# Optimization experiments

Hardware: AMD Instinct MI355X
Metric: run time of the kernel (lower is better)

Reference implementation:

```python
import jax, jax.numpy as jnp
import numpy as np

SEQ, B, IN, H = 1024, 1024, 64, 64

def setup_inputs() -> dict:
    key = jax.random.key(0)
    ks = jax.random.split(key, 6)
    s_in = 1.0 / np.sqrt(IN)
    s_h = 1.0 / np.sqrt(H)
    return {
        "x": jax.random.normal(ks[0], (SEQ, B, IN), dtype=jnp.float32),
        "h": jax.random.normal(ks[1], (1, B, H), dtype=jnp.float32),
        # nn.Linear params: weight (out,in), bias (out,)
        "Wx": jax.random.uniform(ks[2], (H, IN), jnp.float32, -s_in, s_in),
        "bx": jax.random.uniform(ks[3], (H,), jnp.float32, -s_in, s_in),
        "Wh": jax.random.uniform(ks[4], (H, H), jnp.float32, -s_h, s_h),
        "bh": jax.random.uniform(ks[5], (H,), jnp.float32, -s_h, s_h),
    }

def reference(x, h, Wx, bx, Wh, bh):
    act = jnp.tanh  # activation='tanh'
    # Precompute input projection for all timesteps: (S,B,H)
    xp = jnp.einsum('sbi,hi->sbh', x, Wx) + bx
    # lin_h(h).sum(0) with h of shape (1,B,H) == lin_h(h[0])
    h0 = act(jnp.einsum('bj,hj->bh', h[0], Wh) + bh + xp[0])

    def step(h_prev, xt):
        h_new = act(jnp.einsum('bj,hj->bh', h_prev, Wh) + bh + xt)
        return h_new, h_new

    h_last, h_rest = jax.lax.scan(step, h0, xp[1:])
    h_seq = jnp.concatenate([h0[None], h_rest], axis=0)  # (S,B,H)
    return h_seq, h_last
```

## Files before the change

kernel.cpp:

```cpp
#include <hip/hip_runtime.h>
#include <stdint.h>

#define SEQ 1024
#define NB  1024
#define HD  64
#define BH  (NB*HD)
#define RPB 16

typedef _Float16 f16x8 __attribute__((ext_vector_type(8)));
typedef float    f32x4 __attribute__((ext_vector_type(4)));
typedef uint32_t u32x4 __attribute__((ext_vector_type(4)));

#define L2E2 2.8853900817779268f

__device__ __forceinline__ uint32_t pkrtz(float a, float b) {
    auto h = __builtin_amdgcn_cvt_pkrtz(a, b);
    return __builtin_bit_cast(uint32_t, h);
}
__device__ __forceinline__ float tanh_ps(float z) {
    float e = __builtin_amdgcn_exp2f(-__builtin_fabsf(z));
    float a = e + 1.0f;
    float r = __builtin_fmaf(-0.5f, a, 1.45711f);
    r = r * __builtin_fmaf(-a, r, 2.0f);
    r = r * __builtin_fmaf(-a, r, 2.0f);
    float m = __builtin_fmaf(2.0f, r, -1.0f);
    return __builtin_copysignf(m, z);
}
__device__ __forceinline__ void sync_lds() {
    asm volatile("s_waitcnt lgkmcnt(0)" ::: "memory");
    __builtin_amdgcn_s_barrier();
    asm volatile("" ::: "memory");
}

__global__ __launch_bounds__(256, 1) void rnn_kernel(
    const float* __restrict__ x,  const float* __restrict__ h0,
    const float* __restrict__ Wx, const float* __restrict__ bx,
    const float* __restrict__ Wh, const float* __restrict__ bh,
    float* __restrict__ out)
{
    __shared__ uint32_t hw[2][2][4][64];
    __shared__ uint32_t xw[2][2][4][64];

    const int tid  = threadIdx.x;
    const int w    = tid >> 6;
    const int lane = tid & 63;
    const int g    = lane >> 4;
    const int n    = lane & 15;
    const int R0   = blockIdx.x * RPB;
    const size_t row = (size_t)(R0 + n) * HD;
    const size_t xsoff = row + 16 * w + 4 * g;

    f16x8 whA[2], wxA[2];
    #pragma unroll
    for (int T = 0; T < 2; ++T) {
        u32x4 dw, dx;
        #pragma unroll
        for (int q = 0; q < 4; ++q) {
            const int c = 16*q + 4*g + 2*T;
            const float* wp = Wh + (size_t)(16*w + n) * HD + c;
            const float* xr = Wx + (size_t)(16*w + n) * HD + c;
            dw[q] = pkrtz(wp[0]*L2E2, wp[1]*L2E2);
            dx[q] = pkrtz(xr[0]*L2E2, xr[1]*L2E2);
        }
        whA[T] = __builtin_bit_cast(f16x8, dw);
        wxA[T] = __builtin_bit_cast(f16x8, dx);
    }
    f32x4 biasf;
    {
        f32x4 b1 = *(const f32x4*)(bh + 16*w + 4*g);
        f32x4 b2 = *(const f32x4*)(bx + 16*w + 4*g);
        biasf = (b1 + b2) * L2E2;
    }

    {
        f32x4 hv = *(const f32x4*)(h0 + xsoff);
        hw[0][0][w][lane] = pkrtz(hv[0], hv[1]);
        hw[0][1][w][lane] = pkrtz(hv[2], hv[3]);
        f32x4 xv = *(const f32x4*)(x + (size_t)2 * BH + xsoff);
        xw[0][0][w][lane] = pkrtz(xv[0], xv[1]);
        xw[0][1][w][lane] = pkrtz(xv[2], xv[3]);
    }

    f32x4 xp0, xp1;
    #pragma unroll
    for (int s = 0; s < 2; ++s) {
        u32x4 c0, c1;
        #pragma unroll
        for (int q = 0; q < 4; ++q) {
            f32x4 v = *(const f32x4*)(x + (size_t)s * BH + row + 16*q + 4*g);
            c0[q] = pkrtz(v[0], v[1]);
            c1[q] = pkrtz(v[2], v[3]);
        }
        f16x8 f0 = __builtin_bit_cast(f16x8, c0);
        f16x8 f1 = __builtin_bit_cast(f16x8, c1);
        f32x4 tq = __builtin_amdgcn_mfma_f32_16x16x32_f16(wxA[0], f0, biasf, 0, 0, 0);
        f32x4 rv = __builtin_amdgcn_mfma_f32_16x16x32_f16(wxA[1], f1, tq,    0, 0, 0);
        if (s == 0) xp0 = rv; else xp1 = rv;
    }

    f32x4 ring[4];
    ring[3] = *(const f32x4*)(x + (size_t)3 * BH + xsoff);
    ring[0] = *(const f32x4*)(x + (size_t)4 * BH + xsoff);
    ring[1] = *(const f32x4*)(x + (size_t)5 * BH + xsoff);
    ring[2] = *(const f32x4*)(x + (size_t)6 * BH + xsoff);

    const f32x4 zf = {0.f, 0.f, 0.f, 0.f};
    float* optr = out + xsoff;

    sync_lds();

    for (int tb = 0; tb < SEQ; tb += 4) {
        #pragma unroll
        for (int u = 0; u < 4; ++u) {
            const int t = tb + u;
            const int P = u & 1;
            const int Q = (u + 1) & 1;

            u32x4 hc0, hc1, xc0, xc1;
            #pragma unroll
            for (int q = 0; q < 4; ++q) {
                hc0[q] = hw[P][0][q][lane];
                hc1[q] = hw[P][1][q][lane];
                xc0[q] = xw[P][0][q][lane];
                xc1[q] = xw[P][1][q][lane];
            }
            f16x8 fh0 = __builtin_bit_cast(f16x8, hc0);
            f16x8 fh1 = __builtin_bit_cast(f16x8, hc1);
            f16x8 fx0 = __builtin_bit_cast(f16x8, xc0);
            f16x8 fx1 = __builtin_bit_cast(f16x8, xc1);

            f32x4 xpu = (u & 1) ? xp1 : xp0;
            f32x4 pA = __builtin_amdgcn_mfma_f32_16x16x32_f16(whA[0], fh0, xpu, 0, 0, 0);
            f32x4 pB = __builtin_amdgcn_mfma_f32_16x16x32_f16(whA[1], fh1, zf,  0, 0, 0);

            {
                f32x4 tq = __builtin_amdgcn_mfma_f32_16x16x32_f16(wxA[0], fx0, biasf, 0, 0, 0);
                f32x4 rv = __builtin_amdgcn_mfma_f32_16x16x32_f16(wxA[1], fx1, tq,    0, 0, 0);
                if (u & 1) xp1 = rv; else xp0 = rv;
            }

            f32x4 acc = pA + pB;
            f32x4 tv;
            #pragma unroll
            for (int r = 0; r < 4; ++r) tv[r] = tanh_ps(acc[r]);

            hw[Q][0][w][lane] = pkrtz(tv[0], tv[1]);
            hw[Q][1][w][lane] = pkrtz(tv[2], tv[3]);

            {
                f32x4 v = ring[(u + 3) & 3];
                xw[Q][0][w][lane] = pkrtz(v[0], v[1]);
                xw[Q][1][w][lane] = pkrtz(v[2], v[3]);
                int tl = t + 7; tl = tl > SEQ - 1 ? SEQ - 1 : tl;
                ring[(u + 3) & 3] = *(const f32x4*)(x + (size_t)tl * BH + xsoff);
            }

            *(f32x4*)optr = tv;
            if (t == SEQ - 1) *(f32x4*)(optr + BH) = tv;
            optr += BH;

            sync_lds();
        }
    }
}

extern "C" void kernel_launch(void* const* d_in, const int* in_sizes, int n_in,
                              void* d_out, int out_size, void* d_ws, size_t ws_size,
                              hipStream_t stream) {
    const float* x  = (const float*)d_in[0];
    const float* h  = (const float*)d_in[1];
    const float* Wx = (const float*)d_in[2];
    const float* bx = (const float*)d_in[3];
    const float* Wh = (const float*)d_in[4];
    const float* bh = (const float*)d_in[5];
    float* out = (float*)d_out;

    rnn_kernel<<<dim3(NB / RPB), dim3(256), 0, stream>>>(x, h, Wx, bx, Wh, bh, out);
}
```

Baseline: 310.0 us.

## Split recurrence and input-projection into producer/consumer warp groups with LDS handoff

Blocks grow to 512 threads. Four waves run only the recurrent Wh MFMA, tanh and output store. Four producer waves compute the input projection x*Wx+bias ahead of time and pass it through a double-buffered f32 LDS buffer, and the recurrence waves get raised scheduling priority. This removes the Wx MFMAs, x loads and conversions from the critical serial path. The tanh Newton reciprocal is also replaced with a hardware rcp, which costs barrier participation by more waves and an approximate reciprocal.

```diff
diff --git a/kernel.cpp b/kernel.cpp
--- a/kernel.cpp
+++ b/kernel.cpp
@@ -19,10 +19,7 @@
 }
 __device__ __forceinline__ float tanh_ps(float z) {
     float e = __builtin_amdgcn_exp2f(-__builtin_fabsf(z));
-    float a = e + 1.0f;
-    float r = __builtin_fmaf(-0.5f, a, 1.45711f);
-    r = r * __builtin_fmaf(-a, r, 2.0f);
-    r = r * __builtin_fmaf(-a, r, 2.0f);
+    float r = __builtin_amdgcn_rcpf(e + 1.0f);
     float m = __builtin_fmaf(2.0f, r, -1.0f);
     return __builtin_copysignf(m, z);
 }
@@ -32,14 +29,14 @@
     asm volatile("" ::: "memory");
 }
 
-__global__ __launch_bounds__(256, 1) void rnn_kernel(
+__global__ __launch_bounds__(512, 1) void rnn_kernel(
     const float* __restrict__ x,  const float* __restrict__ h0,
     const float* __restrict__ Wx, const float* __restrict__ bx,
     const float* __restrict__ Wh, const float* __restrict__ bh,
     float* __restrict__ out)
 {
     __shared__ uint32_t hw[2][2][4][64];
-    __shared__ uint32_t xw[2][2][4][64];
+    __shared__ __align__(16) f32x4 xpl[2][4][64];
 
     const int tid  = threadIdx.x;
     const int w    = tid >> 6;
@@ -48,118 +45,135 @@
     const int n    = lane & 15;
     const int R0   = blockIdx.x * RPB;
     const size_t row = (size_t)(R0 + n) * HD;
-    const size_t xsoff = row + 16 * w + 4 * g;
 
-    f16x8 whA[2], wxA[2];
-    #pragma unroll
-    for (int T = 0; T < 2; ++T) {
-        u32x4 dw, dx;
+    if (w < 4) {
+        f16x8 whA[2];
         #pragma unroll
-        for (int q = 0; q < 4; ++q) {
-            const int c = 16*q + 4*g + 2*T;
-            const float* wp = Wh + (size_t)(16*w + n) * HD + c;
-            const float* xr = Wx + (size_t)(16*w + n) * HD + c;
-            dw[q] = pkrtz(wp[0]*L2E2, wp[1]*L2E2);
-            dx[q] = pkrtz(xr[0]*L2E2, xr[1]*L2E2);
-        }
-        whA[T] = __builtin_bit_cast(f16x8, dw);
-        wxA[T] = __builtin_bit_cast(f16x8, dx);
-    }
-    f32x4 biasf;
-    {
-        f32x4 b1 = *(const f32x4*)(bh + 16*w + 4*g);
-        f32x4 b2 = *(const f32x4*)(bx + 16*w + 4*g);
-        biasf = (b1 + b2) * L2E2;
-    }
-
-    {
-        f32x4 hv = *(const f32x4*)(h0 + xsoff);
-        hw[0][0][w][lane] = pkrtz(hv[0], hv[1]);
-        hw[0][1][w][lane] = pkrtz(hv[2], hv[3]);
-        f32x4 xv = *(const f32x4*)(x + (size_t)2 * BH + xsoff);
-        xw[0][0][w][lane] = pkrtz(xv[0], xv[1]);
-        xw[0][1][w][lane] = pkrtz(xv[2], xv[3]);
-    }
-
-    f32x4 xp0, xp1;
-    #pragma unroll
-    for (int s = 0; s < 2; ++s) {
-        u32x4 c0, c1;
-        #pragma unroll
-        for (int q = 0; q < 4; ++q) {
-            f32x4 v = *(const f32x4*)(x + (size_t)s * BH + row + 16*q + 4*g);
-            c0[q] = pkrtz(v[0], v[1]);
-            c1[q] = pkrtz(v[2], v[3]);
-        }
-        f16x8 f0 = __builtin_bit_cast(f16x8, c0);
-        f16x8 f1 = __builtin_bit_cast(f16x8, c1);
-        f32x4 tq = __builtin_amdgcn_mfma_f32_16x16x32_f16(wxA[0], f0, biasf, 0, 0, 0);
-        f32x4 rv = __builtin_amdgcn_mfma_f32_16x16x32_f16(wxA[1], f1, tq,    0, 0, 0);
-        if (s == 0) xp0 = rv; else xp1 = rv;
-    }
-
-    f32x4 ring[4];
-    ring[3] = *(const f32x4*)(x + (size_t)3 * BH + xsoff);
-    ring[0] = *(const f32x4*)(x + (size_t)4 * BH + xsoff);
-    ring[1] = *(const f32x4*)(x + (size_t)5 * BH + xsoff);
-    ring[2] = *(const f32x4*)(x + (size_t)6 * BH + xsoff);
-
-    const f32x4 zf = {0.f, 0.f, 0.f, 0.f};
-    float* optr = out + xsoff;
-
-    sync_lds();
-
-    for (int tb = 0; tb < SEQ; tb += 4) {
-        #pragma unroll
-        for (int u = 0; u < 4; ++u) {
-            const int t = tb + u;
-            const int P = u & 1;
-            const int Q = (u + 1) & 1;
-
-            u32x4 hc0, hc1, xc0, xc1;
+        for (int T = 0; T < 2; ++T) {
+            u32x4 dw;
             #pragma unroll
             for (int q = 0; q < 4; ++q) {
-                hc0[q] = hw[P][0][q][lane];
-                hc1[q] = hw[P][1][q][lane];
-                xc0[q] = xw[P][0][q][lane];
-                xc1[q] = xw[P][1][q][lane];
+                const int c = 16*q + 4*g + 2*T;
+                const float* wp = Wh + (size_t)(16*w + n) * HD + c;
+                dw[q] = pkrtz(wp[0]*L2E2, wp[1]*L2E2);
             }
-            f16x8 fh0 = __builtin_bit_cast(f16x8, hc0);
-            f16x8 fh1 = __builtin_bit_cast(f16x8, hc1);
-            f16x8 fx0 = __builtin_bit_cast(f16x8, xc0);
-            f16x8 fx1 = __builtin_bit_cast(f16x8, xc1);
+            whA[T] = __builtin_bit_cast(f16x8, dw);
+        }
+        {
+            f32x4 hv = *(const f32x4*)(h0 + row + 16*w + 4*g);
+            hw[0][0][w][lane] = pkrtz(hv[0], hv[1]);
+            hw[0][1][w][lane] = pkrtz(hv[2], hv[3]);
+        }
+        sync_lds();
+        __builtin_amdgcn_s_setprio(1);
 
-            f32x4 xpu = (u & 1) ? xp1 : xp0;
-            f32x4 pA = __builtin_amdgcn_mfma_f32_16x16x32_f16(whA[0], fh0, xpu, 0, 0, 0);
-            f32x4 pB = __builtin_amdgcn_mfma_f32_16x16x32_f16(whA[1], fh1, zf,  0, 0, 0);
+        const f32x4 zf = {0.f, 0.f, 0.f, 0.f};
+        for (int tb = 0; tb < SEQ; tb += 2) {
+            #pragma unroll
+            for (int u = 0; u < 2; ++u) {
+                const int t = tb + u;
+                const int P = u, Q = u ^ 1;
 
-            {
-                f32x4 tq = __builtin_amdgcn_mfma_f32_16x16x32_f16(wxA[0], fx0, biasf, 0, 0, 0);
-                f32x4 rv = __builtin_amdgcn_mfma_f32_16x16x32_f16(wxA[1], fx1, tq,    0, 0, 0);
-                if (u & 1) xp1 = rv; else xp0 = rv;
+                f32x4 xpC = xpl[P][w][lane];
+                u32x4 hc0, hc1;
+                #pragma unroll
+                for (int q = 0; q < 4; ++q) hc0[q] = hw[P][0][q][lane];
+                #pragma unroll
+                for (int q = 0; q < 4; ++q) hc1[q] = hw[P][1][q][lane];
+                f16x8 fh0 = __builtin_bit_cast(f16x8, hc0);
+                f16x8 fh1 = __builtin_bit_cast(f16x8, hc1);
+
+                f32x4 pA = __builtin_amdgcn_mfma_f32_16x16x32_f16(whA[0], fh0, xpC, 0, 0, 0);
+                f32x4 pB = __builtin_amdgcn_mfma_f32_16x16x32_f16(whA[1], fh1, zf,  0, 0, 0);
+                f32x4 acc = pA + pB;
+
+                f32x4 tv;
+                #pragma unroll
+                for (int r = 0; r < 4; ++r) tv[r] = tanh_ps(acc[r]);
+
+                hw[Q][0][w][lane] = pkrtz(tv[0], tv[1]);
+                hw[Q][1][w][lane] = pkrtz(tv[2], tv[3]);
+
+                {
+                    float* dst = out + (size_t)t * BH + row + 16*w + 4*g;
+                    *(f32x4*)dst = tv;
+                    if (t == SEQ - 1) {
+                        float* dl = out + (size_t)SEQ * BH + row + 16*w + 4*g;
+                        *(f32x4*)dl = tv;
+                    }
+                }
+                sync_lds();
             }
+        }
+    } else {
+        const int p = w - 4;
+        f16x8 wxA[2];
+        #pragma unroll
+        for (int T = 0; T < 2; ++T) {
+            u32x4 dx;
+            #pragma unroll
+            for (int q = 0; q < 4; ++q) {
+                const int c = 16*q + 4*g + 2*T;
+                const float* xr = Wx + (size_t)(16*p + n) * HD + c;
+                dx[q] = pkrtz(xr[0]*L2E2, xr[1]*L2E2);
+            }
+            wxA[T] = __builtin_bit_cast(f16x8, dx);
+        }
+        f32x4 biasf;
+        {
+            f32x4 b1 = *(const f32x4*)(bh + 16*p + 4*g);
+            f32x4 b2 = *(const f32x4*)(bx + 16*p + 4*g);
+            biasf = (b1 + b2) * L2E2;
+        }
+        {
+            u32x4 c0, c1;
+            #pragma unroll
+            for (int q = 0; q < 4; ++q) {
+                f32x4 v = *(const f32x4*)(x + row + 16*q + 4*g);
+                c0[q] = pkrtz(v[0], v[1]);
+                c1[q] = pkrtz(v[2], v[3]);
+            }
+            f16x8 f0 = __builtin_bit_cast(f16x8, c0);
+            f16x8 f1 = __builtin_bit_cast(f16x8, c1);
+            f32x4 tq = __builtin_amdgcn_mfma_f32_16x16x32_f16(wxA[0], f0, biasf, 0, 0, 0);
+            xpl[0][p][lane] = __builtin_amdgcn_mfma_f32_16x16x32_f16(wxA[1], f1, tq, 0, 0, 0);
+        }
+        f32x4 ring[4][4];
+        #pragma unroll
+        for (int s = 1; s <= 4; ++s) {
+            const float* xs = x + (size_t)s * BH + row;
+            #pragma unroll
+            for (int q = 0; q < 4; ++q) ring[s & 3][q] = *(const f32x4*)(xs + 16*q + 4*g);
+        }
+        sync_lds();
 
-            f32x4 acc = pA + pB;
-            f32x4 tv;
+        for (int tb = 0; tb < SEQ; tb += 4) {
             #pragma unroll
-            for (int r = 0; r < 4; ++r) tv[r] = tanh_ps(acc[r]);
+            for (int u = 0; u < 4; ++u) {
+                const int t    = tb + u;
+                const int slot = (u + 1) & 3;
+                const int B    = (u + 1) & 1;
 
-            hw[Q][0][w][lane] = pkrtz(tv[0], tv[1]);
-            hw[Q][1][w][lane] = pkrtz(tv[2], tv[3]);
+                u32x4 c0, c1;
+                #pragma unroll
+                for (int q = 0; q < 4; ++q) {
+                    f32x4 v = ring[slot][q];
+                    c0[q] = pkrtz(v[0], v[1]);
+                    c1[q] = pkrtz(v[2], v[3]);
+                }
+                f16x8 f0 = __builtin_bit_cast(f16x8, c0);
+                f16x8 f1 = __builtin_bit_cast(f16x8, c1);
+                f32x4 tq = __builtin_amdgcn_mfma_f32_16x16x32_f16(wxA[0], f0, biasf, 0, 0, 0);
+                xpl[B][p][lane] = __builtin_amdgcn_mfma_f32_16x16x32_f16(wxA[1], f1, tq, 0, 0, 0);
 
-            {
-                f32x4 v = ring[(u + 3) & 3];
-                xw[Q][0][w][lane] = pkrtz(v[0], v[1]);
-                xw[Q][1][w][lane] = pkrtz(v[2], v[3]);
-                int tl = t + 7; tl = tl > SEQ - 1 ? SEQ - 1 : tl;
-                ring[(u + 3) & 3] = *(const f32x4*)(x + (size_t)tl * BH + xsoff);
+                {
+                    int tl = t + 5; tl = tl > SEQ - 1 ? SEQ - 1 : tl;
+                    const float* xs = x + (size_t)tl * BH + row;
+                    #pragma unroll
+                    for (int q = 0; q < 4; ++q) ring[slot][q] = *(const f32x4*)(xs + 16*q + 4*g);
+                }
+                sync_lds();
             }
-
-            *(f32x4*)optr = tv;
-            if (t == SEQ - 1) *(f32x4*)(optr + BH) = tv;
-            optr += BH;
-
-            sync_lds();
         }
     }
 }
@@ -175,5 +189,5 @@
     const float* bh = (const float*)d_in[5];
     float* out = (float*)d_out;
 
-    rnn_kernel<<<dim3(NB / RPB), dim3(256), 0, stream>>>(x, h, Wx, bx, Wh, bh, out);
+    rnn_kernel<<<dim3(NB / RPB), dim3(512), 0, stream>>>(x, h, Wx, bx, Wh, bh, out);
 }
```

Result: slower. 537.0 us (+73.2%).
